# Performance work log

Hardware: AMD Instinct MI355X
Metric: run time of the kernel (lower is better)

The kernel has to match this reference:

```python
import jax, jax.numpy as jnp
import numpy as np

DIM = 2048
ORDER = 4
L_MAX = 2048
BATCH = 4  # must equal ORDER due to broadcast in the original module
SEQ = 2048


def setup_inputs() -> dict:
    key = jax.random.key(0)
    k1, k2 = jax.random.split(key)
    x = jax.random.normal(k1, (BATCH, DIM, SEQ), dtype=jnp.float32)
    kernel = jax.random.normal(k2, (ORDER, DIM, L_MAX), dtype=jnp.float32) * 0.02
    bias = jnp.zeros((DIM,), dtype=jnp.float32)
    return {"x": x, "kernel": kernel, "bias": bias}


def reference(x, kernel, bias):
    # x: (B, dim, L); kernel: (order, dim, l_max); B == order by broadcast
    seq_len = x.shape[-1]
    n = 2 * seq_len  # zero-padded FFT length for linear (causal) convolution
    x_fft = jnp.fft.rfft(x, n=n, axis=-1)            # (B, dim, n//2+1) complex
    kernel_fft = jnp.fft.rfft(kernel, n=n, axis=-1)  # (order, dim, n//2+1)
    y_fft = x_fft * kernel_fft                       # broadcast: B == order
    y = jnp.fft.irfft(y_fft, n=n, axis=-1)[:, :, :seq_len]
    return y + x + bias[None, :, None]
```

## Files before the change

kernel.cpp:

```cpp
#include <hip/hip_runtime.h>

typedef __attribute__((ext_vector_type(8)))  short short8;
typedef __attribute__((ext_vector_type(16))) float f32x16;
typedef unsigned int uint;

#define SEQ   2048
#define KB0   1024
#define KSTR  1048
#define ZB    (KB0 + 4 * KSTR)
#define LDSU  (ZB + 32)
#define EX0   KB0
#define EX1   (KB0 + 1024)

__device__ inline uint pack2(float lo, float hi_) {
    uint ul = __float_as_uint(lo), uh = __float_as_uint(hi_);
    ul = (ul + 0x7fffu + ((ul >> 16) & 1u)) >> 16;
    uh = (uh + 0x7fffu + ((uh >> 16) & 1u)) >> 16;
    return (ul & 0xffffu) | (uh << 16);
}

__device__ inline int swz(int v) { return v ^ ((v >> 3) & 28); }

#define MFMA(A, B, C) __builtin_amdgcn_mfma_f32_32x32x16_bf16( \
    __builtin_bit_cast(short8, A), __builtin_bit_cast(short8, B), C, 0, 0, 0)

__global__ __launch_bounds__(128, 3)
void hyena_mfma(const float* __restrict__ x, const float* __restrict__ kern,
                const float* __restrict__ bias, float* __restrict__ out)
{
    __shared__ __align__(16) uint lds[LDSU];
    char* ldsb = (char*)lds;

    const int tid = threadIdx.x;
    const int wv  = tid >> 6;
    const int l   = tid & 63;
    const int n   = l & 31;
    const int hi  = l >> 5;
    const int row = blockIdx.x;
    const size_t rb = (size_t)row * SEQ;
    const float bv = bias[row & 2047];

    #pragma unroll
    for (int it = 0; it < 2; ++it) {
        const int e = it * 1024 + 8 * tid;
        float4 a = *(const float4*)&x[rb + e];
        float4 b = *(const float4*)&x[rb + e + 4];
        uint4 w = {pack2(a.x, a.y), pack2(a.z, a.w), pack2(b.x, b.y), pack2(b.z, b.w)};
        *(uint4*)&lds[swz(e >> 1)] = w;
    }

    #pragma unroll
    for (int it = 0; it < 2; ++it) {
        const int j = it * 1024 + 8 * tid;
        const float* kp0 = &kern[rb + (j == 2040 ? 0 : (2036 - j))];
        const float* kp1 = &kern[rb + (2040 - j)];
        float4 f0 = *(const float4*)kp0;
        float4 f1 = *(const float4*)kp1;
        float4 f2 = *(const float4*)(kp1 + 4);
        if (j == 2040) { f0.x = 0.f; f0.y = 0.f; f0.z = 0.f; f0.w = 0.f; }
        const float k0 = f2.w, k1 = f2.z, k2 = f2.y, k3 = f2.x;
        const float k4 = f1.w, k5 = f1.z, k6 = f1.y, k7 = f1.x;
        const float k8 = f0.w, k9 = f0.z, k10 = f0.y;
        const int m = j >> 1;
        uint4 w0 = {pack2(k0,k1), pack2(k2,k3), pack2(k4,k5), pack2(k6,k7)};
        uint4 w1 = {pack2(k1,k2), pack2(k3,k4), pack2(k5,k6), pack2(k7,k8)};
        uint4 w2 = {pack2(k2,k3), pack2(k4,k5), pack2(k6,k7), pack2(k8,k9)};
        uint4 w3 = {pack2(k3,k4), pack2(k5,k6), pack2(k7,k8), pack2(k9,k10)};
        *(uint4*)&lds[KB0 + m]            = w0;
        *(uint4*)&lds[KB0 + KSTR + m]     = w1;
        *(uint4*)&lds[KB0 + 2 * KSTR + m] = w2;
        *(uint4*)&lds[KB0 + 3 * KSTR + m] = w3;
    }
    if (tid < 16) {
        lds[KB0 + 1024 + tid]            = 0u;
        lds[KB0 + KSTR + 1024 + tid]     = 0u;
        lds[KB0 + 2 * KSTR + 1024 + tid] = 0u;
        lds[KB0 + 3 * KSTR + 1024 + tid] = 0u;
    }
    if (tid < 32) lds[ZB + tid] = 0u;
    __syncthreads();

    const int R0   = wv << 4;
    const int st00 = 2047 - n + 8 * hi;
    const int c    = st00 & 3;
    int kb = (KB0 + c * KSTR + ((st00 - c) >> 1)) * 4 - 2048 - (R0 << 6);
    int ua = 16 * n + 4 * hi - (R0 << 4);
    const int zb0 = ZB * 4 + 16 * hi;

    f32x16 acc0 = {}, acc1a = {}, acc1b = {};

    #pragma unroll 2
    for (int i = 0; i < 16; ++i) {
        const int r = R0 + i;
        const int b0  = swz(ua) * 4;
        const int b0s = swz(ua + 8) * 4;
        const int b1  = swz(ua + 512) * 4;
        const int b1s = swz(ua + 520) * 4;
        const int va0  = (n >= r) ? b0  : zb0;
        const int va0s = (n >= r) ? b0s : (zb0 + 32);
        uint4 a00 = *(const uint4*)(ldsb + va0);
        uint4 a01 = *(const uint4*)(ldsb + va0s);
        uint4 a10 = *(const uint4*)(ldsb + b1);
        uint4 a11 = *(const uint4*)(ldsb + b1s);

        uint2 p0 = *(const uint2*)(ldsb + kb + 2048);
        uint2 p1 = *(const uint2*)(ldsb + kb + 2056);
        uint2 p2 = *(const uint2*)(ldsb + kb + 2080);
        uint2 p3 = *(const uint2*)(ldsb + kb + 2088);
        uint2 p4 = *(const uint2*)(ldsb + kb);
        uint2 p5 = *(const uint2*)(ldsb + kb + 8);
        uint2 p6 = *(const uint2*)(ldsb + kb + 32);
        uint2 p7 = *(const uint2*)(ldsb + kb + 40);
        uint4 b00 = {p0.x, p0.y, p1.x, p1.y};
        uint4 b01 = {p2.x, p2.y, p3.x, p3.y};
        uint4 b10 = {p4.x, p4.y, p5.x, p5.y};
        uint4 b11 = {p6.x, p6.y, p7.x, p7.y};

        acc0  = MFMA(a00, b00, acc0);
        acc1a = MFMA(a10, b00, acc1a);
        acc0  = MFMA(a01, b01, acc0);
        acc1a = MFMA(a11, b01, acc1a);
        acc1b = MFMA(a00, b10, acc1b);
        acc1b = MFMA(a01, b11, acc1b);

        ua -= 16;
        kb -= 64;
    }
    __syncthreads();

    f32x16 part_send, part_keep;
    if (wv == 0) { part_send = acc1a + acc1b; part_keep = acc0; }
    else         { part_send = acc0;          part_keep = acc1a + acc1b; }
    const int exw = (wv == 0) ? EX0 : EX1;
    const int exr = (wv == 0) ? EX1 : EX0;
    #pragma unroll
    for (int q = 0; q < 4; ++q) {
        float4 f = {part_send[4*q], part_send[4*q+1], part_send[4*q+2], part_send[4*q+3]};
        *(float4*)&lds[exw + swz(q * 256 + 4 * l)] = f;
    }
    __syncthreads();
    f32x16 tile = part_keep;
    #pragma unroll
    for (int q = 0; q < 4; ++q) {
        float4 f = *(const float4*)&lds[exr + swz(q * 256 + 4 * l)];
        tile[4*q] += f.x; tile[4*q+1] += f.y; tile[4*q+2] += f.z; tile[4*q+3] += f.w;
    }

    const float* xcol = x + rb + n + (size_t)(32 * wv) * 32;
    #pragma unroll
    for (int t = 0; t < 16; ++t) {
        const int rloc = (t & 3) + 8 * (t >> 2) + 4 * hi;
        const int p = 32 * wv + rloc;
        const float xr = xcol[rloc * 32];
        out[rb + (size_t)p * 32 + n] = tile[t] + xr + bv;
    }
}

extern "C" void kernel_launch(void* const* d_in, const int* in_sizes, int n_in,
                              void* d_out, int out_size, void* d_ws, size_t ws_size,
                              hipStream_t stream) {
    const float* x    = (const float*)d_in[0];
    const float* kern = (const float*)d_in[1];
    const float* bias = (const float*)d_in[2];
    float* out = (float*)d_out;

    hipLaunchKernelGGL(hyena_mfma, dim3(4 * 2048), dim3(128), 0, stream,
                       x, kern, bias, out);
}
```

Before: 62.86 us.

## Split MFMA reduction loop across four waves with LDS cross-wave reduction

Doubles block size to 256 threads so four waves each handle half of the Toeplitz row iterations, then reduces partial accumulators across waves through LDS in two phases. The residual x term is now read from the bf16 copy already staged in LDS instead of reloading fp32 from global memory. This aims to raise parallelism and hide MFMA/LDS latency, and to cut global reads. In exchange it adds reduction traffic and barriers, and adds bf16 rounding error to the residual.

```diff
diff --git a/kernel.cpp b/kernel.cpp
--- a/kernel.cpp
+++ b/kernel.cpp
@@ -9,8 +9,7 @@
 #define KSTR  1048
 #define ZB    (KB0 + 4 * KSTR)
 #define LDSU  (ZB + 32)
-#define EX0   KB0
-#define EX1   (KB0 + 1024)
+#define EXB   KB0
 
 __device__ inline uint pack2(float lo, float hi_) {
     uint ul = __float_as_uint(lo), uh = __float_as_uint(hi_);
@@ -24,7 +23,7 @@
 #define MFMA(A, B, C) __builtin_amdgcn_mfma_f32_32x32x16_bf16( \
     __builtin_bit_cast(short8, A), __builtin_bit_cast(short8, B), C, 0, 0, 0)
 
-__global__ __launch_bounds__(128, 3)
+__global__ __launch_bounds__(256, 7)
 void hyena_mfma(const float* __restrict__ x, const float* __restrict__ kern,
                 const float* __restrict__ bias, float* __restrict__ out)
 {
@@ -40,18 +39,15 @@
     const size_t rb = (size_t)row * SEQ;
     const float bv = bias[row & 2047];
 
-    #pragma unroll
-    for (int it = 0; it < 2; ++it) {
-        const int e = it * 1024 + 8 * tid;
+    {
+        const int e = 8 * tid;
         float4 a = *(const float4*)&x[rb + e];
         float4 b = *(const float4*)&x[rb + e + 4];
         uint4 w = {pack2(a.x, a.y), pack2(a.z, a.w), pack2(b.x, b.y), pack2(b.z, b.w)};
         *(uint4*)&lds[swz(e >> 1)] = w;
     }
-
-    #pragma unroll
-    for (int it = 0; it < 2; ++it) {
-        const int j = it * 1024 + 8 * tid;
+    {
+        const int j = 8 * tid;
         const float* kp0 = &kern[rb + (j == 2040 ? 0 : (2036 - j))];
         const float* kp1 = &kern[rb + (2040 - j)];
         float4 f0 = *(const float4*)kp0;
@@ -80,7 +76,7 @@
     if (tid < 32) lds[ZB + tid] = 0u;
     __syncthreads();
 
-    const int R0   = wv << 4;
+    const int R0   = wv << 3;
     const int st00 = 2047 - n + 8 * hi;
     const int c    = st00 & 3;
     int kb = (KB0 + c * KSTR + ((st00 - c) >> 1)) * 4 - 2048 - (R0 << 6);
@@ -90,7 +86,7 @@
     f32x16 acc0 = {}, acc1a = {}, acc1b = {};
 
     #pragma unroll 2
-    for (int i = 0; i < 16; ++i) {
+    for (int i = 0; i < 8; ++i) {
         const int r = R0 + i;
         const int b0  = swz(ua) * 4;
         const int b0s = swz(ua + 8) * 4;
@@ -126,33 +122,47 @@
         ua -= 16;
         kb -= 64;
     }
+    const f32x16 acc1 = acc1a + acc1b;
     __syncthreads();
 
-    f32x16 part_send, part_keep;
-    if (wv == 0) { part_send = acc1a + acc1b; part_keep = acc0; }
-    else         { part_send = acc0;          part_keep = acc1a + acc1b; }
-    const int exw = (wv == 0) ? EX0 : EX1;
-    const int exr = (wv == 0) ? EX1 : EX0;
+    const int m_own = wv & 1, h_own = wv >> 1;
+    float s[8];
     #pragma unroll
-    for (int q = 0; q < 4; ++q) {
-        float4 f = {part_send[4*q], part_send[4*q+1], part_send[4*q+2], part_send[4*q+3]};
-        *(float4*)&lds[exw + swz(q * 256 + 4 * l)] = f;
-    }
-    __syncthreads();
-    f32x16 tile = part_keep;
-    #pragma unroll
-    for (int q = 0; q < 4; ++q) {
-        float4 f = *(const float4*)&lds[exr + swz(q * 256 + 4 * l)];
-        tile[4*q] += f.x; tile[4*q+1] += f.y; tile[4*q+2] += f.z; tile[4*q+3] += f.w;
+    for (int ph = 0; ph < 2; ++ph) {
+        const f32x16& a = ph ? acc1 : acc0;
+        #pragma unroll
+        for (int h = 0; h < 2; ++h)
+            #pragma unroll
+            for (int q2 = 0; q2 < 2; ++q2) {
+                float4 f = {a[8*h+4*q2], a[8*h+4*q2+1], a[8*h+4*q2+2], a[8*h+4*q2+3]};
+                *(float4*)&lds[EXB + (((h * 4 + wv) * 2 + q2) * 64 + l) * 4] = f;
+            }
+        __syncthreads();
+        if (m_own == ph) {
+            #pragma unroll
+            for (int j = 0; j < 8; ++j) s[j] = a[8 * h_own + j];
+            #pragma unroll
+            for (int w = 0; w < 4; ++w) {
+                if (w == wv) continue;
+                #pragma unroll
+                for (int q2 = 0; q2 < 2; ++q2) {
+                    float4 f = *(const float4*)&lds[EXB + (((h_own*4 + w)*2 + q2)*64 + l)*4];
+                    s[4*q2]   += f.x; s[4*q2+1] += f.y;
+                    s[4*q2+2] += f.z; s[4*q2+3] += f.w;
+                }
+            }
+        }
+        __syncthreads();
     }
 
-    const float* xcol = x + rb + n + (size_t)(32 * wv) * 32;
     #pragma unroll
-    for (int t = 0; t < 16; ++t) {
+    for (int t8 = 0; t8 < 8; ++t8) {
+        const int t = 8 * h_own + t8;
         const int rloc = (t & 3) + 8 * (t >> 2) + 4 * hi;
-        const int p = 32 * wv + rloc;
-        const float xr = xcol[rloc * 32];
-        out[rb + (size_t)p * 32 + n] = tile[t] + xr + bv;
+        const int p = 32 * m_own + rloc;
+        const uint w = lds[swz(16 * p + (n >> 1))];
+        const float xr = __uint_as_float((n & 1) ? (w & 0xffff0000u) : (w << 16));
+        out[rb + (size_t)p * 32 + n] = s[t8] + xr + bv;
     }
 }
 
@@ -164,6 +174,6 @@
     const float* bias = (const float*)d_in[2];
     float* out = (float*)d_out;
 
-    hipLaunchKernelGGL(hyena_mfma, dim3(4 * 2048), dim3(128), 0, stream,
+    hipLaunchKernelGGL(hyena_mfma, dim3(4 * 2048), dim3(256), 0, stream,
                        x, kern, bias, out);
 }
```

Result: slower. 74.23 us (+18.1%).

## Halve shifted kernel copies in LDS, raise occupancy, read residual from LDS

Applied to the files above, without the earlier changes.

The kernel now keeps only two parity-shifted bf16 copies of the filter in LDS instead of four, and builds the B fragments from 4-byte-granular reads. This shrinks the LDS footprint enough to raise the launch-bounds occupancy target from 3 to 6 blocks. The exchange buffer drops its swizzle. The residual x term now comes from the bf16 copy already in LDS instead of a second global read. That saves memory traffic but adds bf16 rounding error to the residual path and may produce more, less-aligned LDS reads in the inner loop.

```diff
diff --git a/kernel.cpp b/kernel.cpp
--- a/kernel.cpp
+++ b/kernel.cpp
@@ -6,11 +6,12 @@
 
 #define SEQ   2048
 #define KB0   1024
-#define KSTR  1048
-#define ZB    (KB0 + 4 * KSTR)
-#define LDSU  (ZB + 32)
-#define EX0   KB0
-#define EX1   (KB0 + 1024)
+#define KSTR2 1040
+#define KB1   (KB0 + KSTR2)
+#define ZB    (KB0 + 2 * KSTR2)
+#define LDSU  (ZB + 16)
+#define EX0   1024
+#define EX1   2048
 
 __device__ inline uint pack2(float lo, float hi_) {
     uint ul = __float_as_uint(lo), uh = __float_as_uint(hi_);
@@ -24,7 +25,7 @@
 #define MFMA(A, B, C) __builtin_amdgcn_mfma_f32_32x32x16_bf16( \
     __builtin_bit_cast(short8, A), __builtin_bit_cast(short8, B), C, 0, 0, 0)
 
-__global__ __launch_bounds__(128, 3)
+__global__ __launch_bounds__(128, 6)
 void hyena_mfma(const float* __restrict__ x, const float* __restrict__ kern,
                 const float* __restrict__ bias, float* __restrict__ out)
 {
@@ -48,7 +49,6 @@
         uint4 w = {pack2(a.x, a.y), pack2(a.z, a.w), pack2(b.x, b.y), pack2(b.z, b.w)};
         *(uint4*)&lds[swz(e >> 1)] = w;
     }
-
     #pragma unroll
     for (int it = 0; it < 2; ++it) {
         const int j = it * 1024 + 8 * tid;
@@ -60,30 +60,26 @@
         if (j == 2040) { f0.x = 0.f; f0.y = 0.f; f0.z = 0.f; f0.w = 0.f; }
         const float k0 = f2.w, k1 = f2.z, k2 = f2.y, k3 = f2.x;
         const float k4 = f1.w, k5 = f1.z, k6 = f1.y, k7 = f1.x;
-        const float k8 = f0.w, k9 = f0.z, k10 = f0.y;
+        const float k8 = f0.w;
         const int m = j >> 1;
         uint4 w0 = {pack2(k0,k1), pack2(k2,k3), pack2(k4,k5), pack2(k6,k7)};
         uint4 w1 = {pack2(k1,k2), pack2(k3,k4), pack2(k5,k6), pack2(k7,k8)};
-        uint4 w2 = {pack2(k2,k3), pack2(k4,k5), pack2(k6,k7), pack2(k8,k9)};
-        uint4 w3 = {pack2(k3,k4), pack2(k5,k6), pack2(k7,k8), pack2(k9,k10)};
-        *(uint4*)&lds[KB0 + m]            = w0;
-        *(uint4*)&lds[KB0 + KSTR + m]     = w1;
-        *(uint4*)&lds[KB0 + 2 * KSTR + m] = w2;
-        *(uint4*)&lds[KB0 + 3 * KSTR + m] = w3;
+        *(uint4*)&lds[KB0 + m] = w0;
+        *(uint4*)&lds[KB1 + m] = w1;
     }
     if (tid < 16) {
-        lds[KB0 + 1024 + tid]            = 0u;
-        lds[KB0 + KSTR + 1024 + tid]     = 0u;
-        lds[KB0 + 2 * KSTR + 1024 + tid] = 0u;
-        lds[KB0 + 3 * KSTR + 1024 + tid] = 0u;
+        lds[KB0 + 1024 + tid] = 0u;
+        lds[KB1 + 1024 + tid] = 0u;
+        lds[ZB + tid] = 0u;
     }
-    if (tid < 32) lds[ZB + tid] = 0u;
     __syncthreads();
 
     const int R0   = wv << 4;
     const int st00 = 2047 - n + 8 * hi;
-    const int c    = st00 & 3;
-    int kb = (KB0 + c * KSTR + ((st00 - c) >> 1)) * 4 - 2048 - (R0 << 6);
+    const int par  = st00 & 1;
+    int kb  = (KB0 + par * KSTR2 + (st00 >> 1)) * 4 - 2048 - (R0 << 6);
+    int kbh = kb + 2048;
+    asm volatile("" : "+v"(kbh));
     int ua = 16 * n + 4 * hi - (R0 << 4);
     const int zb0 = ZB * 4 + 16 * hi;
 
@@ -103,18 +99,12 @@
         uint4 a10 = *(const uint4*)(ldsb + b1);
         uint4 a11 = *(const uint4*)(ldsb + b1s);
 
-        uint2 p0 = *(const uint2*)(ldsb + kb + 2048);
-        uint2 p1 = *(const uint2*)(ldsb + kb + 2056);
-        uint2 p2 = *(const uint2*)(ldsb + kb + 2080);
-        uint2 p3 = *(const uint2*)(ldsb + kb + 2088);
-        uint2 p4 = *(const uint2*)(ldsb + kb);
-        uint2 p5 = *(const uint2*)(ldsb + kb + 8);
-        uint2 p6 = *(const uint2*)(ldsb + kb + 32);
-        uint2 p7 = *(const uint2*)(ldsb + kb + 40);
-        uint4 b00 = {p0.x, p0.y, p1.x, p1.y};
-        uint4 b01 = {p2.x, p2.y, p3.x, p3.y};
-        uint4 b10 = {p4.x, p4.y, p5.x, p5.y};
-        uint4 b11 = {p6.x, p6.y, p7.x, p7.y};
+        const uint* kl = (const uint*)(ldsb + kb);
+        const uint* kh = (const uint*)(ldsb + kbh);
+        uint4 b00 = {kh[0], kh[1], kh[2],  kh[3]};
+        uint4 b01 = {kh[8], kh[9], kh[10], kh[11]};
+        uint4 b10 = {kl[0], kl[1], kl[2],  kl[3]};
+        uint4 b11 = {kl[8], kl[9], kl[10], kl[11]};
 
         acc0  = MFMA(a00, b00, acc0);
         acc1a = MFMA(a10, b00, acc1a);
@@ -123,8 +113,9 @@
         acc1b = MFMA(a00, b10, acc1b);
         acc1b = MFMA(a01, b11, acc1b);
 
-        ua -= 16;
-        kb -= 64;
+        ua  -= 16;
+        kb  -= 64;
+        kbh -= 64;
     }
     __syncthreads();
 
@@ -136,22 +127,22 @@
     #pragma unroll
     for (int q = 0; q < 4; ++q) {
         float4 f = {part_send[4*q], part_send[4*q+1], part_send[4*q+2], part_send[4*q+3]};
-        *(float4*)&lds[exw + swz(q * 256 + 4 * l)] = f;
+        *(float4*)&lds[exw + q * 256 + 4 * l] = f;
     }
     __syncthreads();
     f32x16 tile = part_keep;
     #pragma unroll
     for (int q = 0; q < 4; ++q) {
-        float4 f = *(const float4*)&lds[exr + swz(q * 256 + 4 * l)];
+        float4 f = *(const float4*)&lds[exr + q * 256 + 4 * l];
         tile[4*q] += f.x; tile[4*q+1] += f.y; tile[4*q+2] += f.z; tile[4*q+3] += f.w;
     }
 
-    const float* xcol = x + rb + n + (size_t)(32 * wv) * 32;
     #pragma unroll
     for (int t = 0; t < 16; ++t) {
         const int rloc = (t & 3) + 8 * (t >> 2) + 4 * hi;
         const int p = 32 * wv + rloc;
-        const float xr = xcol[rloc * 32];
+        const uint w = lds[swz(16 * p + (n >> 1))];
+        const float xr = __uint_as_float((n & 1) ? (w & 0xffff0000u) : (w << 16));
         out[rb + (size_t)p * 32 + n] = tile[t] + xr + bv;
     }
 }
```

Result: faster. 60.50 us (-3.8%).
